# Kernel optimization log

Measured on AMD Instinct MI355X. Metric: run time of the kernel, lower is better.

## Reference

```python
import jax, jax.numpy as jnp
import numpy as np

NEG = -9e15

def setup_inputs() -> dict:
    key = jax.random.key(0)
    k1, k2, k3, k4 = jax.random.split(key, 4)
    N, Fin, Fout = 8192, 256, 256
    h = jax.random.normal(k1, (N, Fin), dtype=jnp.float32)
    adj = jax.random.randint(k2, (N, N), 0, 2).astype(jnp.float32)
    W = jax.random.normal(k3, (Fin, Fout), dtype=jnp.float32) * (1.414 * np.sqrt(2.0 / (Fin + Fout)))
    a = jax.random.normal(k4, (2 * Fout, 1), dtype=jnp.float32) * (1.414 * np.sqrt(2.0 / (2 * Fout + 1)))
    return {"h": h, "adj": adj, "W": W, "a": a}

def reference(h, adj, W, a):
    Fout = W.shape[1]
    Wh = h @ W                                  # [N, Fout]
    Wh1 = Wh @ a[:Fout, :]                      # [N, 1]
    Wh2 = Wh @ a[Fout:, :]                      # [N, 1]
    e = jax.nn.leaky_relu(Wh1 + Wh2.T, 0.2)     # [N, N]
    mask = (adj > 0).astype(e.dtype)
    e = e * mask + NEG * (1.0 - mask)
    attention = jax.nn.softmax(e, axis=1)       # [N, N]
    h_prime = attention @ Wh                    # [N, Fout]
    return jax.nn.elu(h_prime)
```

## Files before the change

kernel.cpp:

```cpp
#include <hip/hip_runtime.h>
#include <hip/hip_bf16.h>
#include <stdint.h>

typedef __attribute__((ext_vector_type(4))) short short4v;
typedef __attribute__((ext_vector_type(8))) short short8v;
typedef __attribute__((ext_vector_type(4))) float float4v;

#define NN 8192
#define FIN 256
#define FOUT 256

__device__ __forceinline__ short f2bf(float f) {
    unsigned u = __float_as_uint(f);
    unsigned r = u + 0x7fffu + ((u >> 16) & 1u);
    return (short)(r >> 16);
}

__global__ __launch_bounds__(256) void k_wt(const float* __restrict__ W, short* __restrict__ WT) {
    int k = blockIdx.x, n = threadIdx.x;
    WT[n * 256 + k] = f2bf(W[k * 256 + n]);
}

__global__ __launch_bounds__(256) void k_gemm1(const float* __restrict__ h, const short* __restrict__ WT,
                                               float* __restrict__ Wh) {
    __shared__ short sA[64 * 40];
    __shared__ short sB[64 * 40];
    int bm = blockIdx.x;
    int bn = blockIdx.y;
    int t  = threadIdx.x;
    int w = t >> 6, lane = t & 63, quad = lane >> 4, l16 = lane & 15;

    float4v acc[4];
#pragma unroll
    for (int c = 0; c < 4; c++)
#pragma unroll
        for (int j = 0; j < 4; j++) acc[c][j] = 0.f;

    int r  = t >> 2;
    int ko = (t & 3) * 8;

    for (int k0 = 0; k0 < 256; k0 += 32) {
        const float4v* src = (const float4v*)&h[(size_t)(64 * bm + r) * 256 + k0 + ko];
        float4v v0 = src[0], v1 = src[1];
        short8v pk;
        pk[0] = f2bf(v0[0]); pk[1] = f2bf(v0[1]); pk[2] = f2bf(v0[2]); pk[3] = f2bf(v0[3]);
        pk[4] = f2bf(v1[0]); pk[5] = f2bf(v1[1]); pk[6] = f2bf(v1[2]); pk[7] = f2bf(v1[3]);
        *(short8v*)&sA[r * 40 + ko] = pk;
        short8v bv = *(const short8v*)&WT[(size_t)(64 * bn + r) * 256 + k0 + ko];
        *(short8v*)&sB[r * 40 + ko] = bv;
        __syncthreads();

        short8v af = *(const short8v*)&sA[(16 * w + l16) * 40 + quad * 8];
#pragma unroll
        for (int c = 0; c < 4; c++) {
            short8v bf = *(const short8v*)&sB[(16 * c + l16) * 40 + quad * 8];
            acc[c] = __builtin_amdgcn_mfma_f32_16x16x32_bf16(af, bf, acc[c], 0, 0, 0);
        }
        __syncthreads();
    }
#pragma unroll
    for (int c = 0; c < 4; c++)
#pragma unroll
        for (int j = 0; j < 4; j++) {
            int row = 64 * bm + 16 * w + quad * 4 + j;
            int col = 64 * bn + 16 * c + l16;
            Wh[(size_t)row * 256 + col] = acc[c][j];
        }
}

__global__ __launch_bounds__(256) void k_rowstats(const float* __restrict__ Wh, const float* __restrict__ a,
                                                  float* __restrict__ Wh1, float* __restrict__ Wh2,
                                                  unsigned* __restrict__ maxenc) {
    int w = threadIdx.x >> 6, lane = threadIdx.x & 63;
    int row = blockIdx.x * 4 + w;
    float s1 = 0.f, s2 = 0.f;
#pragma unroll
    for (int j = 0; j < 4; j++) {
        int c = lane + 64 * j;
        float v = Wh[(size_t)row * 256 + c];
        s1 += v * a[c];
        s2 += v * a[256 + c];
    }
#pragma unroll
    for (int off = 32; off; off >>= 1) {
        s1 += __shfl_down(s1, off);
        s2 += __shfl_down(s2, off);
    }
    if (lane == 0) {
        Wh1[row] = s1;
        Wh2[row] = s2;
        unsigned u = __float_as_uint(s2);
        unsigned key = (u & 0x80000000u) ? ~u : (u | 0x80000000u);
        atomicMax(maxenc, key);
    }
}

__global__ __launch_bounds__(256) void k_transpose(const float* __restrict__ Wh, short* __restrict__ WhT) {
    __shared__ short sT[64 * 72];
    int bm = blockIdx.x, bn = blockIdx.y;
    int t = threadIdx.x;
#pragma unroll
    for (int i = 0; i < 4; i++) {
        int idx = i * 256 + t;
        int r = idx >> 4, c4 = (idx & 15) * 4;
        float4v v = *(const float4v*)&Wh[(size_t)(64 * bm + r) * 256 + 64 * bn + c4];
#pragma unroll
        for (int j = 0; j < 4; j++) sT[(c4 + j) * 72 + r] = f2bf(v[j]);
    }
    __syncthreads();
    int c = t >> 2, ro = (t & 3) * 16;
#pragma unroll
    for (int hh = 0; hh < 2; hh++) {
        short8v v = *(const short8v*)&sT[c * 72 + ro + 8 * hh];
        *(short8v*)&WhT[(size_t)(64 * bn + c) * 8192 + 64 * bm + ro + 8 * hh] = v;
    }
}

__global__ __launch_bounds__(512, 4) void k_gat(const float* __restrict__ adj, const short* __restrict__ WhT,
                                                const float* __restrict__ Wh1, const float* __restrict__ Wh2,
                                                const unsigned* __restrict__ maxenc,
                                                float* __restrict__ Cacc, float* __restrict__ Lacc,
                                                int Ksub) {
    __shared__ short sB[2][256 * 64];
    __shared__ short sA[64 * 72];
    int bm = blockIdx.x;
    int sidx = blockIdx.y;
    int kb = sidx * Ksub;
    int t = threadIdx.x;
    int lane = t & 63, quad = lane >> 4, l16 = lane & 15;
    int w = t >> 6;
    int mr = (w >> 2) * 32;
    int cg = w & 3;

    unsigned key = maxenc[0];
    unsigned u = (key & 0x80000000u) ? (key & 0x7fffffffu) : ~key;
    float maxw2 = __uint_as_float(u);

    int r  = t >> 3;
    int kc = (t & 7) * 8;
    float wh1r = Wh1[64 * bm + r];
    float sup = wh1r + maxw2;
    float ci = fmaxf(sup, 0.2f * sup);

    const float* adj_row = &adj[(size_t)(64 * bm + r) * 8192 + kb];
    const float* w2base  = &Wh2[kb];

    int schunk = (t & 7) ^ ((t >> 3) & 7);
    const short* gb0 = &WhT[(size_t)(t >> 3) * 8192 + kb + schunk * 8];
    short* sBbase = &sB[0][0];

    float4v acc[2][4];
#pragma unroll
    for (int rt = 0; rt < 2; rt++)
#pragma unroll
        for (int c = 0; c < 4; c++)
#pragma unroll
            for (int j = 0; j < 4; j++) acc[rt][c][j] = 0.f;
    float lsum = 0.f;

#pragma unroll
    for (int i = 0; i < 4; i++)
        __builtin_amdgcn_global_load_lds(
            (const __attribute__((address_space(1))) void*)(gb0 + (size_t)i * 64 * 8192),
            (__attribute__((address_space(3))) void*)(sBbase + t * 8 + i * 512 * 8),
            16, 0, 0);
    float4v av0 = *(const float4v*)&adj_row[kc];
    float4v av1 = *(const float4v*)&adj_row[kc + 4];
    float4v w20 = *(const float4v*)&w2base[kc];
    float4v w21 = *(const float4v*)&w2base[kc + 4];
    float4v bv0, bv1, x20, x21;

    auto body = [&](int k0, int curbuf,
                    float4v& AV0, float4v& AV1, float4v& W20, float4v& W21,
                    float4v& NAV0, float4v& NAV1, float4v& NW20, float4v& NW21) {
        int k0n = k0 + 64;
        if (k0n < Ksub) {
            short* lb = sBbase + (curbuf ^ 1) * (256 * 64) + t * 8;
            const short* gs = gb0 + k0n;
#pragma unroll
            for (int i = 0; i < 4; i++)
                __builtin_amdgcn_global_load_lds(
                    (const __attribute__((address_space(1))) void*)(gs + (size_t)i * 64 * 8192),
                    (__attribute__((address_space(3))) void*)(lb + i * 512 * 8),
                    16, 0, 0);
            NAV0 = *(const float4v*)&adj_row[k0n + kc];
            NAV1 = *(const float4v*)&adj_row[k0n + kc + 4];
            NW20 = *(const float4v*)&w2base[k0n + kc];
            NW21 = *(const float4v*)&w2base[k0n + kc + 4];
        }
        short8v pk;
#pragma unroll
        for (int j = 0; j < 4; j++) {
            float s = wh1r + W20[j];
            float f = fmaxf(s, 0.2f * s);
            float p = __expf(f - ci);
            p = (AV0[j] > 0.f) ? p : 0.f;
            lsum += p;
            pk[j] = f2bf(p);
        }
#pragma unroll
        for (int j = 0; j < 4; j++) {
            float s = wh1r + W21[j];
            float f = fmaxf(s, 0.2f * s);
            float p = __expf(f - ci);
            p = (AV1[j] > 0.f) ? p : 0.f;
            lsum += p;
            pk[4 + j] = f2bf(p);
        }
        *(short8v*)&sA[r * 72 + kc] = pk;
        if (k0n < Ksub) asm volatile("s_waitcnt vmcnt(8) lgkmcnt(0)" ::: "memory");
        else            asm volatile("s_waitcnt vmcnt(0) lgkmcnt(0)" ::: "memory");
        __builtin_amdgcn_s_barrier();
        __builtin_amdgcn_s_setprio(1);
        const short* sBc = sBbase + curbuf * (256 * 64);
#pragma unroll
        for (int kk = 0; kk < 2; kk++) {
            short8v af0 = *(const short8v*)&sA[(mr + l16) * 72 + kk * 32 + quad * 8];
            short8v af1 = *(const short8v*)&sA[(mr + 16 + l16) * 72 + kk * 32 + quad * 8];
#pragma unroll
            for (int c = 0; c < 4; c++) {
                int n = 64 * cg + 16 * c + l16;
                int ch = (kk * 4 + quad) ^ (n & 7);
                short8v bf = *(const short8v*)&sBc[n * 64 + ch * 8];
                acc[0][c] = __builtin_amdgcn_mfma_f32_16x16x32_bf16(af0, bf, acc[0][c], 0, 0, 0);
                acc[1][c] = __builtin_amdgcn_mfma_f32_16x16x32_bf16(af1, bf, acc[1][c], 0, 0, 0);
            }
        }
        __builtin_amdgcn_s_setprio(0);
        __builtin_amdgcn_s_barrier();
    };

    for (int k0 = 0; k0 < Ksub; k0 += 128) {
        body(k0,      0, av0, av1, w20, w21, bv0, bv1, x20, x21);
        body(k0 + 64, 1, bv0, bv1, x20, x21, av0, av1, w20, w21);
    }

#pragma unroll
    for (int off = 4; off; off >>= 1) lsum += __shfl_xor(lsum, off, 8);
    if ((t & 7) == 0) atomicAdd(&Lacc[64 * bm + r], lsum);

#pragma unroll
    for (int rt = 0; rt < 2; rt++)
#pragma unroll
        for (int c = 0; c < 4; c++)
#pragma unroll
            for (int j = 0; j < 4; j++) {
                int row = 64 * bm + mr + rt * 16 + quad * 4 + j;
                int col = 64 * cg + 16 * c + l16;
                atomicAdd(&Cacc[(size_t)row * 256 + col], acc[rt][c][j]);
            }
}

__global__ __launch_bounds__(256) void k_final(const float* __restrict__ Cacc, const float* __restrict__ Lacc,
                                               float* __restrict__ out) {
    int idx = blockIdx.x * 256 + threadIdx.x;
    int row = idx >> 6;
    int c4 = (idx & 63) * 4;
    float4v v = *(const float4v*)&Cacc[(size_t)row * 256 + c4];
    float inv = 1.0f / fmaxf(Lacc[row], 1e-30f);
    float4v o;
#pragma unroll
    for (int j = 0; j < 4; j++) {
        float x = v[j] * inv;
        o[j] = (x > 0.f) ? x : (__expf(x) - 1.f);
    }
    *(float4v*)&out[(size_t)row * 256 + c4] = o;
}

extern "C" void kernel_launch(void* const* d_in, const int* in_sizes, int n_in,
                              void* d_out, int out_size, void* d_ws, size_t ws_size,
                              hipStream_t stream) {
    const float* h   = (const float*)d_in[0];
    const float* adj = (const float*)d_in[1];
    const float* W   = (const float*)d_in[2];
    const float* a   = (const float*)d_in[3];
    float* out = (float*)d_out;

    const int S = 4;
    const int Ksub = NN / S;

    char* ws = (char*)d_ws;
    float*    Wh     = (float*)(ws);
    float*    Cacc   = (float*)(ws);
    short*    WhT    = (short*)(ws + 8388608);
    char*     tail   = ws + 12582912;
    short*    WT     = (short*)(tail);
    float*    Wh1    = (float*)(tail + 131072);
    float*    Wh2    = (float*)(tail + 163840);
    float*    Lacc   = (float*)(tail + 196608);
    unsigned* maxenc = (unsigned*)(tail + 229376);

    hipMemsetAsync(maxenc, 0, sizeof(unsigned), stream);

    k_wt<<<256, 256, 0, stream>>>(W, WT);
    k_gemm1<<<dim3(128, 4), 256, 0, stream>>>(h, WT, Wh);
    k_rowstats<<<2048, 256, 0, stream>>>(Wh, a, Wh1, Wh2, maxenc);
    k_transpose<<<dim3(128, 4), 256, 0, stream>>>(Wh, WhT);
    hipMemsetAsync(Cacc, 0, (size_t)NN * 256 * sizeof(float), stream);
    hipMemsetAsync(Lacc, 0, (size_t)NN * sizeof(float), stream);
    k_gat<<<dim3(128, S), 512, 0, stream>>>(adj, WhT, Wh1, Wh2, maxenc, Cacc, Lacc, Ksub);
    k_final<<<2048, 256, 0, stream>>>(Cacc, Lacc, out);
}
```

Before: 541.0 us.

## Stage WhT tiles through registers with two-ahead prefetch instead of direct LDS loads

Replaces the asynchronous global-to-LDS loads of the WhT tile with ordinary vector loads into registers. Each tile is fetched two iterations ahead and written into the alternate XOR-swizzled LDS buffer one iteration ahead. The explicit vmcnt waits are dropped, leaving only an lgkmcnt wait before the barrier, so the compiler now places the memory waits. This aims to decouple B-tile fetch latency from the barrier, but it costs extra VGPRs and extra LDS store instructions, and may lower occupancy.

```diff
diff --git a/kernel.cpp b/kernel.cpp
--- a/kernel.cpp
+++ b/kernel.cpp
@@ -145,9 +145,10 @@
     const float* adj_row = &adj[(size_t)(64 * bm + r) * 8192 + kb];
     const float* w2base  = &Wh2[kb];
 
-    int schunk = (t & 7) ^ ((t >> 3) & 7);
-    const short* gb0 = &WhT[(size_t)(t >> 3) * 8192 + kb + schunk * 8];
-    short* sBbase = &sB[0][0];
+    int nrow = t >> 1;
+    int half = t & 1;
+    const short* gB = &WhT[(size_t)nrow * 8192 + kb + half * 32];
+    int nx = nrow & 7;
 
     float4v acc[2][4];
 #pragma unroll
@@ -158,35 +159,41 @@
             for (int j = 0; j < 4; j++) acc[rt][c][j] = 0.f;
     float lsum = 0.f;
 
-#pragma unroll
-    for (int i = 0; i < 4; i++)
-        __builtin_amdgcn_global_load_lds(
-            (const __attribute__((address_space(1))) void*)(gb0 + (size_t)i * 64 * 8192),
-            (__attribute__((address_space(3))) void*)(sBbase + t * 8 + i * 512 * 8),
-            16, 0, 0);
-    float4v av0 = *(const float4v*)&adj_row[kc];
-    float4v av1 = *(const float4v*)&adj_row[kc + 4];
-    float4v w20 = *(const float4v*)&w2base[kc];
-    float4v w21 = *(const float4v*)&w2base[kc + 4];
+    short8v rA[4], rB[4];
+    float4v av0, av1, w20, w21;
     float4v bv0, bv1, x20, x21;
 
-    auto body = [&](int k0, int curbuf,
+    av0 = *(const float4v*)&adj_row[kc];
+    av1 = *(const float4v*)&adj_row[kc + 4];
+    w20 = *(const float4v*)&w2base[kc];
+    w21 = *(const float4v*)&w2base[kc + 4];
+#pragma unroll
+    for (int j = 0; j < 4; j++) rA[j] = *(const short8v*)&gB[(size_t)j * 8];
+#pragma unroll
+    for (int j = 0; j < 4; j++)
+        *(short8v*)&sB[0][nrow * 64 + (((half * 4 + j) ^ nx)) * 8] = rA[j];
+#pragma unroll
+    for (int j = 0; j < 4; j++) rB[j] = *(const short8v*)&gB[64 + (size_t)j * 8];
+
+    auto body = [&](int k0, int cur,
                     float4v& AV0, float4v& AV1, float4v& W20, float4v& W21,
-                    float4v& NAV0, float4v& NAV1, float4v& NW20, float4v& NW21) {
-        int k0n = k0 + 64;
-        if (k0n < Ksub) {
-            short* lb = sBbase + (curbuf ^ 1) * (256 * 64) + t * 8;
-            const short* gs = gb0 + k0n;
-#pragma unroll
-            for (int i = 0; i < 4; i++)
-                __builtin_amdgcn_global_load_lds(
-                    (const __attribute__((address_space(1))) void*)(gs + (size_t)i * 64 * 8192),
-                    (__attribute__((address_space(3))) void*)(lb + i * 512 * 8),
-                    16, 0, 0);
-            NAV0 = *(const float4v*)&adj_row[k0n + kc];
-            NAV1 = *(const float4v*)&adj_row[k0n + kc + 4];
-            NW20 = *(const float4v*)&w2base[k0n + kc];
-            NW21 = *(const float4v*)&w2base[k0n + kc + 4];
+                    float4v& NAV0, float4v& NAV1, float4v& NW20, float4v& NW21,
+                    short8v (&rCur)[4], short8v (&rNext)[4]) {
+        int k1 = k0 + 64, k2 = k0 + 128;
+        if (k1 < Ksub) {
+            NAV0 = *(const float4v*)&adj_row[k1 + kc];
+            NAV1 = *(const float4v*)&adj_row[k1 + kc + 4];
+            NW20 = *(const float4v*)&w2base[k1 + kc];
+            NW21 = *(const float4v*)&w2base[k1 + kc + 4];
+        }
+        if (k2 < Ksub) {
+#pragma unroll
+            for (int j = 0; j < 4; j++) rNext[j] = *(const short8v*)&gB[k2 + (size_t)j * 8];
+        }
+        if (k1 < Ksub) {
+#pragma unroll
+            for (int j = 0; j < 4; j++)
+                *(short8v*)&sB[cur ^ 1][nrow * 64 + (((half * 4 + j) ^ nx)) * 8] = rCur[j];
         }
         short8v pk;
 #pragma unroll
@@ -208,11 +215,10 @@
             pk[4 + j] = f2bf(p);
         }
         *(short8v*)&sA[r * 72 + kc] = pk;
-        if (k0n < Ksub) asm volatile("s_waitcnt vmcnt(8) lgkmcnt(0)" ::: "memory");
-        else            asm volatile("s_waitcnt vmcnt(0) lgkmcnt(0)" ::: "memory");
+        asm volatile("s_waitcnt lgkmcnt(0)" ::: "memory");
         __builtin_amdgcn_s_barrier();
         __builtin_amdgcn_s_setprio(1);
-        const short* sBc = sBbase + curbuf * (256 * 64);
+        const short* sBc = &sB[cur][0];
 #pragma unroll
         for (int kk = 0; kk < 2; kk++) {
             short8v af0 = *(const short8v*)&sA[(mr + l16) * 72 + kk * 32 + quad * 8];
@@ -231,8 +237,8 @@
     };
 
     for (int k0 = 0; k0 < Ksub; k0 += 128) {
-        body(k0,      0, av0, av1, w20, w21, bv0, bv1, x20, x21);
-        body(k0 + 64, 1, bv0, bv1, x20, x21, av0, av1, w20, w21);
+        body(k0,      0, av0, av1, w20, w21, bv0, bv1, x20, x21, rB, rA);
+        body(k0 + 64, 1, bv0, bv1, x20, x21, av0, av1, w20, w21, rA, rB);
     }
 
 #pragma unroll
```

Result: slower. 665.6 us (+23.0%).
